# Optimization experiments

Measured on AMD Instinct MI355X. Metric: run time of the kernel, lower is better.

Reference implementation:

```python
import jax, jax.numpy as jnp
import numpy as np

EPS = 1e-8


def setup_inputs() -> dict:
    key = jax.random.key(0)
    k1, k2 = jax.random.split(key)
    latent = jax.random.normal(k1, (16, 192, 64, 64), dtype=jnp.float32)
    codebook = jax.random.normal(k2, (1024, 192), dtype=jnp.float32)
    # codebook rows are unit-normalized at init in the original module
    codebook = codebook / jnp.linalg.norm(codebook, axis=-1, keepdims=True)
    return {"latent": latent, "codebook": codebook}


def reference(latent, codebook):
    b, c, h, w = latent.shape
    # [B,C,H,W] -> [N, C]
    x = jnp.transpose(latent, (0, 2, 3, 1)).reshape(-1, c)
    x = x / (jnp.linalg.norm(x, axis=-1, keepdims=True) + EPS)
    x2 = jnp.sum(x * x, axis=-1, keepdims=True)            # [N,1]
    c2 = jnp.sum(codebook * codebook, axis=-1)             # [K]
    dist_sq = x2 - 2.0 * jnp.einsum('nd,kd->nk', x, codebook) + c2[None, :]
    indices = jnp.argmin(dist_sq, axis=-1)                 # [N]
    quantized_flat = codebook[indices]                     # [N,C] gather
    quantized = jnp.transpose(quantized_flat.reshape(b, h, w, c), (0, 3, 1, 2))
    return quantized, indices.reshape(b, h, w)
```

## Files before the change

kernel.cpp:

```cpp
#include <hip/hip_runtime.h>
#include <hip/hip_bf16.h>


#define NPTS   65536
#define DIMS   192
#define KCB    1024
#define HW     4096
#define QELEMS 12582912

typedef __attribute__((ext_vector_type(8))) _Float16 f16x8;
typedef __attribute__((ext_vector_type(4))) _Float16 f16x4;
typedef __attribute__((ext_vector_type(4))) float f32x4;

#define MARGIN_Q 4864u

__device__ __forceinline__ void async_load16(const void* g, void* l) {
    __builtin_amdgcn_global_load_lds(
        (const __attribute__((address_space(1))) unsigned int*)g,
        (__attribute__((address_space(3))) unsigned int*)l, 16, 0, 0);
}

__device__ __forceinline__ unsigned qdist(float d) {
    float t = (d + 1.0f) * 1048576.0f;
    t = fminf(fmaxf(t, 0.0f), 4194303.0f);
    return (unsigned)t;
}

__device__ __forceinline__ void top2_merge(unsigned& b, unsigned& s,
                                           unsigned ob, unsigned os) {
    unsigned nb = min(b, ob);
    unsigned ns = min(max(b, ob), min(s, os));
    b = nb; s = ns;
}

__global__ __launch_bounds__(256) void k_prep_cb16(const float* __restrict__ cbk,
                                                   _Float16* __restrict__ Bpf) {
    int id = blockIdx.x * 256 + threadIdx.x;
    if (id >= KCB * DIMS) return;
    int k = id / DIMS, d = id % DIMS;
    Bpf[((size_t)(d >> 6) * KCB + k) * 64 + (d & 63)] = (_Float16)cbk[id];
}

__global__ __launch_bounds__(256) void k_c2(const float* __restrict__ cbk,
                                            float* __restrict__ c2) {
    int k = blockIdx.x * 256 + threadIdx.x;
    if (k >= KCB) return;
    const float4* row = (const float4*)(cbk + (size_t)k * DIMS);
    float s = 0.f;
    #pragma unroll
    for (int i = 0; i < DIMS / 4; ++i) {
        float4 v = row[i];
        s += v.x * v.x + v.y * v.y + v.z * v.z + v.w * v.w;
    }
    c2[k] = s;
}

__global__ __launch_bounds__(256) void k_cbT(const float* __restrict__ cbk,
                                             float* __restrict__ cbkT) {
    __shared__ float q[64 * 193];
    const int tid = threadIdx.x;
    const int k0 = blockIdx.x * 64;
    const int lane = tid & 63;
    const int grp = tid >> 6;
    for (int r = grp; r < 64; r += 4) {
        const float* row = cbk + (size_t)(k0 + r) * DIMS;
        for (int c = lane; c < DIMS; c += 64) q[r * 193 + c] = row[c];
    }
    __syncthreads();
    for (int d = grp; d < DIMS; d += 4) {
        cbkT[(size_t)d * KCB + k0 + lane] = q[lane * 193 + d];
    }
}

__global__ __launch_bounds__(256, 2) void k_gemm_f(const float* __restrict__ latent,
                                                   const _Float16* __restrict__ Bpf,
                                                   const float* __restrict__ c2,
                                                   const float* __restrict__ cbk,
                                                   float* __restrict__ out_q,
                                                   float* __restrict__ idxf,
                                                   int* __restrict__ list,
                                                   int* __restrict__ cnt) {
    __shared__ __align__(16) _Float16 As[128 * 200];
    __shared__ __align__(16) _Float16 Bs[128 * 64];
    __shared__ float inv_s[128];
    __shared__ uint2 t2buf[256];
    __shared__ int sidx[128];

    const int tid = threadIdx.x;
    const int wave = tid >> 6;
    const int lane = tid & 63;
    const int quad = lane >> 4;
    const int l15 = lane & 15;
    const int wm = (wave >> 1) * 64;
    const int wn = (wave & 1) * 64;
    const int n0 = blockIdx.x * 128;
    const int bB = n0 >> 12;
    const int hw0 = n0 & 4095;

    {
        float* part = (float*)Bs;
        const float* lat = latent + (size_t)bB * DIMS * HW + hw0;
        const int p = tid & 127, ch = tid >> 7;
        float ss = 0.f;
        #pragma unroll 4
        for (int i = 0; i < 24; ++i) {
            int c0 = i * 8 + ch * 4;
            float v0 = lat[(size_t)(c0 + 0) * HW + p];
            float v1 = lat[(size_t)(c0 + 1) * HW + p];
            float v2 = lat[(size_t)(c0 + 2) * HW + p];
            float v3 = lat[(size_t)(c0 + 3) * HW + p];
            ss = fmaf(v0, v0, fmaf(v1, v1, fmaf(v2, v2, fmaf(v3, v3, ss))));
            f16x4 h = { (_Float16)v0, (_Float16)v1, (_Float16)v2, (_Float16)v3 };
            *(f16x4*)&As[p * 200 + c0] = h;
        }
        part[ch * 128 + p] = ss;
        __syncthreads();
        if (tid < 128)
            inv_s[tid] = 1.0f / (sqrtf(part[tid] + part[128 + tid]) + 1e-8f);
        __syncthreads();
    }

    unsigned rb[16], rs[16];
    #pragma unroll
    for (int i = 0; i < 16; ++i) { rb[i] = 0xFFFFFFFFu; rs[i] = 0xFFFFFFFFu; }

    for (int nb = 0; nb < 8; ++nb) {
        f32x4 acc[4][4];
        #pragma unroll
        for (int mt = 0; mt < 4; ++mt)
            #pragma unroll
            for (int nt = 0; nt < 4; ++nt)
                #pragma unroll
                for (int r = 0; r < 4; ++r) acc[mt][nt][r] = 0.f;

        for (int g = 0; g < 3; ++g) {
            __syncthreads();
            #pragma unroll
            for (int i = 0; i < 4; ++i) {
                int u = i * 256 + tid;
                int m = u >> 3, c = u & 7;
                int sw = c ^ (m & 7);
                async_load16(Bpf + (((size_t)g * KCB + nb * 128 + m) * 8 + sw) * 8,
                             &Bs[u * 8]);
            }
            __syncthreads();
            #pragma unroll
            for (int s = 0; s < 2; ++s) {
                f16x8 af[4], bfr[4];
                #pragma unroll
                for (int mt = 0; mt < 4; ++mt) {
                    int m = wm + mt * 16 + l15;
                    af[mt] = *(const f16x8*)&As[m * 200 + g * 64 + s * 32 + quad * 8];
                }
                #pragma unroll
                for (int nt = 0; nt < 4; ++nt) {
                    int n = wn + nt * 16 + l15;
                    int c = (s * 4 + quad) ^ (n & 7);
                    bfr[nt] = *(const f16x8*)&Bs[n * 64 + c * 8];
                }
                #pragma unroll
                for (int mt = 0; mt < 4; ++mt)
                    #pragma unroll
                    for (int nt = 0; nt < 4; ++nt)
                        acc[mt][nt] = __builtin_amdgcn_mfma_f32_16x16x32_f16(
                            af[mt], bfr[nt], acc[mt][nt], 0, 0, 0);
            }
        }

        int kbase = nb * 128 + wn;
        float c2v[4];
        #pragma unroll
        for (int nt = 0; nt < 4; ++nt) c2v[nt] = c2[kbase + nt * 16 + l15];
        #pragma unroll
        for (int mt = 0; mt < 4; ++mt) {
            #pragma unroll
            for (int r = 0; r < 4; ++r) {
                float inv = inv_s[wm + mt * 16 + quad * 4 + r];
                unsigned p[4];
                #pragma unroll
                for (int nt = 0; nt < 4; ++nt) {
                    float dist = fmaf(-2.f * inv, acc[mt][nt][r], c2v[nt]);
                    p[nt] = (qdist(dist) << 10) | (unsigned)(kbase + nt * 16 + l15);
                }
                unsigned b01 = min(p[0], p[1]), s01 = max(p[0], p[1]);
                unsigned b23 = min(p[2], p[3]), s23 = max(p[2], p[3]);
                unsigned nbb = min(b01, b23);
                unsigned nbs = min(max(b01, b23), min(s01, s23));
                top2_merge(rb[mt * 4 + r], rs[mt * 4 + r], nbb, nbs);
            }
        }
    }

    __syncthreads();
    #pragma unroll
    for (int i = 0; i < 16; ++i) {
        unsigned b = rb[i], s = rs[i];
        #pragma unroll
        for (int off = 1; off < 16; off <<= 1) {
            unsigned ob = __shfl_xor(b, off, 64);
            unsigned os = __shfl_xor(s, off, 64);
            top2_merge(b, s, ob, os);
        }
        if (l15 == 0) {
            int mt = i >> 2, r = i & 3;
            int mloc = wm + mt * 16 + quad * 4 + r;
            t2buf[mloc * 2 + (wave & 1)] = make_uint2(b, s);
        }
    }
    __syncthreads();
    if (tid < 128) {
        uint2 x = t2buf[tid * 2];
        uint2 y = t2buf[tid * 2 + 1];
        unsigned b = x.x, s = x.y;
        top2_merge(b, s, y.x, y.y);
        int k = (int)(b & 1023u);
        sidx[tid] = k;
        idxf[n0 + tid] = (float)k;
        if (((s >> 10) - (b >> 10)) < MARGIN_Q) {
            int pos = atomicAdd(cnt, 1);
            list[pos] = n0 + tid;
        }
    }
    __syncthreads();

    float* q = (float*)As;
    for (int chk = 0; chk < 4; ++chk) {
        int p0 = chk * 32;
        for (int r = wave; r < 32; r += 4) {
            const float* row = cbk + (size_t)sidx[p0 + r] * DIMS;
            for (int c = lane; c < DIMS; c += 64) q[r * 193 + c] = row[c];
        }
        __syncthreads();
        float* ob = out_q + (size_t)bB * DIMS * HW + hw0 + p0;
        #pragma unroll
        for (int i = 0; i < 24; ++i) {
            int u = i * 256 + tid;
            int c = u >> 5, p = u & 31;
            ob[(size_t)c * HW + p] = q[p * 193 + c];
        }
        __syncthreads();
    }
}

__global__ __launch_bounds__(256) void k_rescore16(const float* __restrict__ latent,
                                                   const float* __restrict__ cbkT,
                                                   const float* __restrict__ cbk,
                                                   const float* __restrict__ c2,
                                                   const int* __restrict__ list,
                                                   const int* __restrict__ cnt,
                                                   float* __restrict__ out_q,
                                                   float* __restrict__ idxf) {
    __shared__ float xs[16][200];
    __shared__ float part[16][16];
    __shared__ float inv_s[16];
    __shared__ unsigned long long best[16];
    const int tid = threadIdx.x;
    const int count = *cnt;
    const float4* ct = (const float4*)cbkT;
    const int j = tid >> 4, dl = tid & 15;

    for (int base = blockIdx.x * 16; base < count; base += gridDim.x * 16) {
        __syncthreads();
        float ss = 0.f;
        int n = 0, bb = 0, hw = 0;
        bool valid = (base + j) < count;
        if (valid) {
            n = list[base + j]; bb = n >> 12; hw = n & 4095;
            #pragma unroll
            for (int i = 0; i < 12; ++i) {
                int d = dl + i * 16;
                float v = latent[((size_t)bb * DIMS + d) * HW + hw];
                xs[j][d] = v;
                ss = fmaf(v, v, ss);
            }
        }
        part[j][dl] = ss;
        if (tid < 16) best[tid] = ~0ull;
        __syncthreads();
        if (tid < 16) {
            float s = 0.f;
            #pragma unroll
            for (int i = 0; i < 16; ++i) s += part[tid][i];
            inv_s[tid] = 1.0f / (sqrtf(s) + 1e-8f);
        }
        __syncthreads();

        float4 a[16];
        #pragma unroll
        for (int p = 0; p < 16; ++p) a[p] = make_float4(0.f, 0.f, 0.f, 0.f);
        for (int d = 0; d < DIMS; d += 4) {
            float4 cv0 = ct[(size_t)(d + 0) * 256 + tid];
            float4 cv1 = ct[(size_t)(d + 1) * 256 + tid];
            float4 cv2 = ct[(size_t)(d + 2) * 256 + tid];
            float4 cv3 = ct[(size_t)(d + 3) * 256 + tid];
            #pragma unroll
            for (int p = 0; p < 16; ++p) {
                float4 xv = *(const float4*)&xs[p][d];
                a[p].x = fmaf(xv.x, cv0.x, a[p].x); a[p].y = fmaf(xv.x, cv0.y, a[p].y);
                a[p].z = fmaf(xv.x, cv0.z, a[p].z); a[p].w = fmaf(xv.x, cv0.w, a[p].w);
                a[p].x = fmaf(xv.y, cv1.x, a[p].x); a[p].y = fmaf(xv.y, cv1.y, a[p].y);
                a[p].z = fmaf(xv.y, cv1.z, a[p].z); a[p].w = fmaf(xv.y, cv1.w, a[p].w);
                a[p].x = fmaf(xv.z, cv2.x, a[p].x); a[p].y = fmaf(xv.z, cv2.y, a[p].y);
                a[p].z = fmaf(xv.z, cv2.z, a[p].z); a[p].w = fmaf(xv.z, cv2.w, a[p].w);
                a[p].x = fmaf(xv.w, cv3.x, a[p].x); a[p].y = fmaf(xv.w, cv3.y, a[p].y);
                a[p].z = fmaf(xv.w, cv3.z, a[p].z); a[p].w = fmaf(xv.w, cv3.w, a[p].w);
            }
        }
        #pragma unroll
        for (int p = 0; p < 16; ++p) {
            float inv = inv_s[p];
            float dot4[4] = {a[p].x, a[p].y, a[p].z, a[p].w};
            unsigned long long loc = ~0ull;
            #pragma unroll
            for (int e = 0; e < 4; ++e) {
                int k = 4 * tid + e;
                float dist = c2[k] - 2.f * inv * dot4[e];
                unsigned ub = __float_as_uint(dist);
                ub ^= (ub >> 31) ? 0xFFFFFFFFu : 0x80000000u;
                unsigned long long pk =
                    ((unsigned long long)ub << 32) | (unsigned)k;
                loc = loc < pk ? loc : pk;
            }
            #pragma unroll
            for (int off = 1; off < 64; off <<= 1) {
                unsigned long long o = __shfl_xor(loc, off, 64);
                loc = loc < o ? loc : o;
            }
            if ((tid & 63) == 0) atomicMin(&best[p], loc);
        }
        __syncthreads();
        if (valid) {
            int kk = (int)(best[j] & 0xFFFFFFFFull);
            #pragma unroll
            for (int i = 0; i < 12; ++i) {
                int d = dl + i * 16;
                out_q[((size_t)bb * DIMS + d) * HW + hw] = cbk[(size_t)kk * DIMS + d];
            }
            if (dl == 0) idxf[n] = (float)kk;
        }
    }
}

__global__ __launch_bounds__(256) void k_norms_fb(const float* __restrict__ latent,
                                                  float* __restrict__ inv_norm) {
    __shared__ float red[256];
    const int tid = threadIdx.x;
    const int n0 = blockIdx.x * 128;
    const int nl = tid & 127;
    const int half = tid >> 7;
    const int b = n0 >> 12;
    const int hw = (n0 & 4095) + nl;
    const float* base = latent + (size_t)b * DIMS * HW + hw;
    float ssq = 0.f;
    for (int c = half; c < DIMS; c += 2) {
        float v = base[(size_t)c * HW];
        ssq = fmaf(v, v, ssq);
    }
    red[tid] = ssq;
    __syncthreads();
    if (half == 0) {
        float s = red[tid] + red[tid + 128];
        inv_norm[n0 + nl] = 1.0f / (sqrtf(s) + 1e-8f);
    }
}

#define LDX  132
__global__ __launch_bounds__(256) void k_dist_fb(const float* __restrict__ latent,
                                                 const float* __restrict__ cbk,
                                                 const float* __restrict__ inv_norm,
                                                 const float* __restrict__ c2,
                                                 int* __restrict__ idx_out,
                                                 float* __restrict__ idxf_out) {
    __shared__ __align__(16) float xsm[64 * LDX];
    __shared__ __align__(16) float csm[64 * LDX];
    __shared__ unsigned long long red[128];
    const int tid = threadIdx.x;
    const int n0 = blockIdx.x * 128;
    const int b = n0 >> 12;
    const int hw0 = n0 & 4095;
    const int kt = tid & 15;
    const int mt = tid >> 4;
    const float* lat_base = latent + (size_t)b * DIMS * HW + hw0;
    float inv[8];
    #pragma unroll
    for (int i = 0; i < 8; ++i) inv[i] = inv_norm[n0 + mt * 8 + i];
    float best[8];
    int bidx[8];
    #pragma unroll
    for (int i = 0; i < 8; ++i) { best[i] = 3.4e38f; bidx[i] = 0; }
    const int nl = tid & 127;
    const int cp = tid >> 7;
    for (int k0 = 0; k0 < KCB; k0 += 128) {
        float acc[8][8];
        #pragma unroll
        for (int i = 0; i < 8; ++i)
            #pragma unroll
            for (int j = 0; j < 8; ++j) acc[i][j] = 0.f;
        for (int d0 = 0; d0 < DIMS; d0 += 64) {
            __syncthreads();
            for (int cc = cp; cc < 64; cc += 2)
                xsm[cc * LDX + nl] = lat_base[(size_t)(d0 + cc) * HW + nl];
            #pragma unroll
            for (int i = 0; i < 8; ++i) {
                int f4 = tid + 256 * i;
                int kk = f4 >> 4;
                int dq = f4 & 15;
                float4 v = *(const float4*)(cbk + (size_t)(k0 + kk) * DIMS + d0 + dq * 4);
                csm[(dq * 4 + 0) * LDX + kk] = v.x;
                csm[(dq * 4 + 1) * LDX + kk] = v.y;
                csm[(dq * 4 + 2) * LDX + kk] = v.z;
                csm[(dq * 4 + 3) * LDX + kk] = v.w;
            }
            __syncthreads();
            for (int d = 0; d < 64; ++d) {
                const float* xr = &xsm[d * LDX + mt * 8];
                const float* cr = &csm[d * LDX + kt * 8];
                float x8[8], c8[8];
                *(float4*)&x8[0] = *(const float4*)&xr[0];
                *(float4*)&x8[4] = *(const float4*)&xr[4];
                *(float4*)&c8[0] = *(const float4*)&cr[0];
                *(float4*)&c8[4] = *(const float4*)&cr[4];
                #pragma unroll
                for (int i = 0; i < 8; ++i)
                    #pragma unroll
                    for (int j = 0; j < 8; ++j)
                        acc[i][j] = fmaf(x8[i], c8[j], acc[i][j]);
            }
        }
        float cc2[8];
        #pragma unroll
        for (int j = 0; j < 8; ++j) cc2[j] = c2[k0 + kt * 8 + j];
        #pragma unroll
        for (int i = 0; i < 8; ++i)
            #pragma unroll
            for (int j = 0; j < 8; ++j) {
                float t = inv[i] * acc[i][j];
                float dist = fmaf(-2.f, t, cc2[j]);
                int kidx = k0 + kt * 8 + j;
                if (dist < best[i]) { best[i] = dist; bidx[i] = kidx; }
            }
    }
    if (tid < 128) red[tid] = ~0ull;
    __syncthreads();
    #pragma unroll
    for (int i = 0; i < 8; ++i) {
        unsigned long long p =
            ((unsigned long long)__float_as_uint(best[i]) << 32) | (unsigned)bidx[i];
        atomicMin(&red[mt * 8 + i], p);
    }
    __syncthreads();
    if (tid < 128) {
        int k = (int)(red[tid] & 0xFFFFFFFFu);
        idx_out[n0 + tid] = k;
        idxf_out[n0 + tid] = (float)k;
    }
}

__global__ __launch_bounds__(256) void k_gather(const float* __restrict__ cbk,
                                                const int* __restrict__ idx,
                                                float* __restrict__ out) {
    __shared__ float q[64 * 193];
    __shared__ int sidx[64];
    const int tid = threadIdx.x;
    const int n0 = blockIdx.x * 64;
    const int b = n0 >> 12;
    const int hw0 = n0 & 4095;
    const int lane = tid & 63;
    const int grp = tid >> 6;

    if (tid < 64) sidx[tid] = idx[n0 + tid];
    __syncthreads();
    for (int r = grp; r < 64; r += 4) {
        const float* row = cbk + (size_t)sidx[r] * DIMS;
        for (int c = lane; c < DIMS; c += 64) q[r * 193 + c] = row[c];
    }
    __syncthreads();
    float* obase = out + (size_t)b * DIMS * HW + hw0;
    for (int c = grp; c < DIMS; c += 4) {
        obase[(size_t)c * HW + lane] = q[lane * 193 + c];
    }
}

extern "C" void kernel_launch(void* const* d_in, const int* in_sizes, int n_in,
                              void* d_out, int out_size, void* d_ws, size_t ws_size,
                              hipStream_t stream) {
    const float* latent = (const float*)d_in[0];
    const float* cbk = (const float*)d_in[1];
    float* out = (float*)d_out;
    float* out_q = out;
    float* out_idx = out + QELEMS;

    if (ws_size >= 2u * 1024u * 1024u) {
        char* w = (char*)d_ws;
        _Float16* Bpf = (_Float16*)w;
        float* cbkT = (float*)(w + 393216);
        float* c2 = (float*)(w + 1179648);
        int* list = (int*)(w + 1183744);
        int* cnt = (int*)(w + 1445888);

        hipMemsetAsync(cnt, 0, 4, stream);
        k_prep_cb16<<<768, 256, 0, stream>>>(cbk, Bpf);
        k_c2<<<4, 256, 0, stream>>>(cbk, c2);
        k_cbT<<<KCB / 64, 256, 0, stream>>>(cbk, cbkT);
        k_gemm_f<<<512, 256, 0, stream>>>(latent, Bpf, c2, cbk, out_q, out_idx,
                                          list, cnt);
        k_rescore16<<<512, 256, 0, stream>>>(latent, cbkT, cbk, c2, list, cnt,
                                             out_q, out_idx);
    } else {
        float* inv_norm = (float*)d_ws;
        float* c2 = inv_norm + NPTS;
        int* idx = (int*)(c2 + KCB);
        k_norms_fb<<<NPTS / 128, 256, 0, stream>>>(latent, inv_norm);
        k_c2<<<4, 256, 0, stream>>>(cbk, c2);
        k_dist_fb<<<NPTS / 128, 256, 0, stream>>>(latent, cbk, inv_norm, c2, idx, out_idx);
        k_gather<<<NPTS / 64, 256, 0, stream>>>(cbk, idx, out_q);
    }
}
```

Before: 234.7 us.

## Double-buffer codebook tiles, keep A fragments in registers, score by max dot product

The GEMM main loop is restructured. Codebook tiles are now 32-wide K-chunks loaded asynchronously into a double-buffered LDS area, so the next chunk's load overlaps with the current MFMAs and each step needs fewer barriers. The A fragments for all six chunks are preloaded into registers once. Scoring drops the c2 term and argmaxes the scaled dot product, which assumes unit-norm codebook rows. The rescoring margin is halved to shrink the candidate list, at the cost of more register pressure and a reliance on the unit-norm property.

```diff
diff --git a/kernel.cpp b/kernel.cpp
--- a/kernel.cpp
+++ b/kernel.cpp
@@ -1,5 +1,4 @@
 #include <hip/hip_runtime.h>
-#include <hip/hip_bf16.h>
 
 
 #define NPTS   65536
@@ -12,7 +11,7 @@
 typedef __attribute__((ext_vector_type(4))) _Float16 f16x4;
 typedef __attribute__((ext_vector_type(4))) float f32x4;
 
-#define MARGIN_Q 4864u
+#define MARGIN_Q 2432u
 
 __device__ __forceinline__ void async_load16(const void* g, void* l) {
     __builtin_amdgcn_global_load_lds(
@@ -20,16 +19,10 @@
         (__attribute__((address_space(3))) unsigned int*)l, 16, 0, 0);
 }
 
-__device__ __forceinline__ unsigned qdist(float d) {
-    float t = (d + 1.0f) * 1048576.0f;
-    t = fminf(fmaxf(t, 0.0f), 4194303.0f);
-    return (unsigned)t;
-}
-
-__device__ __forceinline__ void top2_merge(unsigned& b, unsigned& s,
-                                           unsigned ob, unsigned os) {
-    unsigned nb = min(b, ob);
-    unsigned ns = min(max(b, ob), min(s, os));
+__device__ __forceinline__ void top2_merge_max(unsigned& b, unsigned& s,
+                                               unsigned ob, unsigned os) {
+    unsigned nb = max(b, ob);
+    unsigned ns = max(min(b, ob), max(s, os));
     b = nb; s = ns;
 }
 
@@ -38,7 +31,7 @@
     int id = blockIdx.x * 256 + threadIdx.x;
     if (id >= KCB * DIMS) return;
     int k = id / DIMS, d = id % DIMS;
-    Bpf[((size_t)(d >> 6) * KCB + k) * 64 + (d & 63)] = (_Float16)cbk[id];
+    Bpf[((size_t)(d >> 5) * KCB + k) * 32 + (d & 31)] = (_Float16)cbk[id];
 }
 
 __global__ __launch_bounds__(256) void k_c2(const float* __restrict__ cbk,
@@ -74,14 +67,13 @@
 
 __global__ __launch_bounds__(256, 2) void k_gemm_f(const float* __restrict__ latent,
                                                    const _Float16* __restrict__ Bpf,
-                                                   const float* __restrict__ c2,
                                                    const float* __restrict__ cbk,
                                                    float* __restrict__ out_q,
                                                    float* __restrict__ idxf,
                                                    int* __restrict__ list,
                                                    int* __restrict__ cnt) {
     __shared__ __align__(16) _Float16 As[128 * 200];
-    __shared__ __align__(16) _Float16 Bs[128 * 64];
+    __shared__ __align__(16) _Float16 Bs[2][128 * 32];
     __shared__ float inv_s[128];
     __shared__ uint2 t2buf[256];
     __shared__ int sidx[128];
@@ -98,7 +90,7 @@
     const int hw0 = n0 & 4095;
 
     {
-        float* part = (float*)Bs;
+        float* part = (float*)&Bs[0][0];
         const float* lat = latent + (size_t)bB * DIMS * HW + hw0;
         const int p = tid & 127, ch = tid >> 7;
         float ss = 0.f;
@@ -120,9 +112,42 @@
         __syncthreads();
     }
 
+    f16x8 af[6][4];
+    #pragma unroll
+    for (int c = 0; c < 6; ++c)
+        #pragma unroll
+        for (int mt = 0; mt < 4; ++mt)
+            af[c][mt] = *(const f16x8*)&As[(wm + mt * 16 + l15) * 200 + c * 32 + quad * 8];
+
+    float scl[16];
+    #pragma unroll
+    for (int mt = 0; mt < 4; ++mt)
+        #pragma unroll
+        for (int r = 0; r < 4; ++r)
+            scl[mt * 4 + r] = inv_s[wm + mt * 16 + quad * 4 + r] * 1048576.0f;
+
     unsigned rb[16], rs[16];
     #pragma unroll
-    for (int i = 0; i < 16; ++i) { rb[i] = 0xFFFFFFFFu; rs[i] = 0xFFFFFFFFu; }
+    for (int i = 0; i < 16; ++i) { rb[i] = 0u; rs[i] = 0u; }
+
+    int kn[4];
+    #pragma unroll
+    for (int nt = 0; nt < 4; ++nt) kn[nt] = wn + nt * 16 + l15;
+
+    const int u0 = tid, u1 = tid + 256;
+    const int pu0 = (u0 & ~3) | ((u0 & 3) ^ ((u0 >> 2) & 3));
+    const int pu1 = (u1 & ~3) | ((u1 & 3) ^ ((u1 >> 2) & 3));
+    const int bfo = (wn + l15) * 32 + ((quad ^ (l15 & 3)) * 8);
+
+    {
+        const _Float16* s0 = Bpf;
+        async_load16(s0 + (size_t)pu0 * 8, &Bs[0][u0 * 8]);
+        async_load16(s0 + (size_t)pu1 * 8, &Bs[0][u1 * 8]);
+        const _Float16* s1 = Bpf + (size_t)KCB * 32;
+        async_load16(s1 + (size_t)pu0 * 8, &Bs[1][u0 * 8]);
+        async_load16(s1 + (size_t)pu1 * 8, &Bs[1][u1 * 8]);
+    }
+    int nb_s = 0, c_s = 2;
 
     for (int nb = 0; nb < 8; ++nb) {
         f32x4 acc[4][4];
@@ -133,62 +158,53 @@
                 #pragma unroll
                 for (int r = 0; r < 4; ++r) acc[mt][nt][r] = 0.f;
 
-        for (int g = 0; g < 3; ++g) {
-            __syncthreads();
-            #pragma unroll
-            for (int i = 0; i < 4; ++i) {
-                int u = i * 256 + tid;
-                int m = u >> 3, c = u & 7;
-                int sw = c ^ (m & 7);
-                async_load16(Bpf + (((size_t)g * KCB + nb * 128 + m) * 8 + sw) * 8,
-                             &Bs[u * 8]);
-            }
-            __syncthreads();
-            #pragma unroll
-            for (int s = 0; s < 2; ++s) {
-                f16x8 af[4], bfr[4];
+        #pragma unroll
+        for (int c = 0; c < 6; ++c) {
+            if (c == 5 && nb == 7) {
+                asm volatile("s_waitcnt vmcnt(0)" ::: "memory");
+            } else {
+                asm volatile("s_waitcnt vmcnt(2)" ::: "memory");
+            }
+            __builtin_amdgcn_s_barrier();
+            const int buf = (nb * 6 + c) & 1;
+            f16x8 bf[4];
+            #pragma unroll
+            for (int nt = 0; nt < 4; ++nt)
+                bf[nt] = *(const f16x8*)&Bs[buf][bfo + nt * 512];
+            #pragma unroll
+            for (int mt = 0; mt < 4; ++mt)
                 #pragma unroll
-                for (int mt = 0; mt < 4; ++mt) {
-                    int m = wm + mt * 16 + l15;
-                    af[mt] = *(const f16x8*)&As[m * 200 + g * 64 + s * 32 + quad * 8];
-                }
-                #pragma unroll
-                for (int nt = 0; nt < 4; ++nt) {
-                    int n = wn + nt * 16 + l15;
-                    int c = (s * 4 + quad) ^ (n & 7);
-                    bfr[nt] = *(const f16x8*)&Bs[n * 64 + c * 8];
-                }
-                #pragma unroll
-                for (int mt = 0; mt < 4; ++mt)
-                    #pragma unroll
-                    for (int nt = 0; nt < 4; ++nt)
-                        acc[mt][nt] = __builtin_amdgcn_mfma_f32_16x16x32_f16(
-                            af[mt], bfr[nt], acc[mt][nt], 0, 0, 0);
-            }
-        }
-
-        int kbase = nb * 128 + wn;
-        float c2v[4];
-        #pragma unroll
-        for (int nt = 0; nt < 4; ++nt) c2v[nt] = c2[kbase + nt * 16 + l15];
+                for (int nt = 0; nt < 4; ++nt)
+                    acc[mt][nt] = __builtin_amdgcn_mfma_f32_16x16x32_f16(
+                        af[c][mt], bf[nt], acc[mt][nt], 0, 0, 0);
+            asm volatile("s_waitcnt lgkmcnt(0)" ::: "memory");
+            __builtin_amdgcn_s_barrier();
+            if (!((c >= 4) && nb == 7)) {
+                const _Float16* src = Bpf + ((size_t)c_s * KCB + nb_s * 128) * 32;
+                async_load16(src + (size_t)pu0 * 8, &Bs[buf][u0 * 8]);
+                async_load16(src + (size_t)pu1 * 8, &Bs[buf][u1 * 8]);
+                if (++c_s == 6) { c_s = 0; ++nb_s; }
+            }
+        }
+
         #pragma unroll
         for (int mt = 0; mt < 4; ++mt) {
             #pragma unroll
             for (int r = 0; r < 4; ++r) {
-                float inv = inv_s[wm + mt * 16 + quad * 4 + r];
-                unsigned p[4];
-                #pragma unroll
-                for (int nt = 0; nt < 4; ++nt) {
-                    float dist = fmaf(-2.f * inv, acc[mt][nt][r], c2v[nt]);
-                    p[nt] = (qdist(dist) << 10) | (unsigned)(kbase + nt * 16 + l15);
-                }
-                unsigned b01 = min(p[0], p[1]), s01 = max(p[0], p[1]);
-                unsigned b23 = min(p[2], p[3]), s23 = max(p[2], p[3]);
-                unsigned nbb = min(b01, b23);
-                unsigned nbs = min(max(b01, b23), min(s01, s23));
-                top2_merge(rb[mt * 4 + r], rs[mt * 4 + r], nbb, nbs);
-            }
-        }
+                float sc = scl[mt * 4 + r];
+                unsigned p0 = ((unsigned)fmaf(acc[mt][0][r], sc, 2097152.0f) << 10) | (unsigned)kn[0];
+                unsigned p1 = ((unsigned)fmaf(acc[mt][1][r], sc, 2097152.0f) << 10) | (unsigned)kn[1];
+                unsigned p2 = ((unsigned)fmaf(acc[mt][2][r], sc, 2097152.0f) << 10) | (unsigned)kn[2];
+                unsigned p3 = ((unsigned)fmaf(acc[mt][3][r], sc, 2097152.0f) << 10) | (unsigned)kn[3];
+                unsigned b01 = max(p0, p1), s01 = min(p0, p1);
+                unsigned b23 = max(p2, p3), s23 = min(p2, p3);
+                unsigned bb = max(b01, b23);
+                unsigned s4 = max(min(b01, b23), max(s01, s23));
+                top2_merge_max(rb[mt * 4 + r], rs[mt * 4 + r], bb, s4);
+            }
+        }
+        #pragma unroll
+        for (int nt = 0; nt < 4; ++nt) kn[nt] += 128;
     }
 
     __syncthreads();
@@ -199,7 +215,7 @@
         for (int off = 1; off < 16; off <<= 1) {
             unsigned ob = __shfl_xor(b, off, 64);
             unsigned os = __shfl_xor(s, off, 64);
-            top2_merge(b, s, ob, os);
+            top2_merge_max(b, s, ob, os);
         }
         if (l15 == 0) {
             int mt = i >> 2, r = i & 3;
@@ -212,11 +228,11 @@
         uint2 x = t2buf[tid * 2];
         uint2 y = t2buf[tid * 2 + 1];
         unsigned b = x.x, s = x.y;
-        top2_merge(b, s, y.x, y.y);
+        top2_merge_max(b, s, y.x, y.y);
         int k = (int)(b & 1023u);
         sidx[tid] = k;
         idxf[n0 + tid] = (float)k;
-        if (((s >> 10) - (b >> 10)) < MARGIN_Q) {
+        if (((b >> 10) - (s >> 10)) < MARGIN_Q) {
             int pos = atomicAdd(cnt, 1);
             list[pos] = n0 + tid;
         }
@@ -502,7 +518,7 @@
         k_prep_cb16<<<768, 256, 0, stream>>>(cbk, Bpf);
         k_c2<<<4, 256, 0, stream>>>(cbk, c2);
         k_cbT<<<KCB / 64, 256, 0, stream>>>(cbk, cbkT);
-        k_gemm_f<<<512, 256, 0, stream>>>(latent, Bpf, c2, cbk, out_q, out_idx,
+        k_gemm_f<<<512, 256, 0, stream>>>(latent, Bpf, cbk, out_q, out_idx,
                                           list, cnt);
         k_rescore16<<<512, 256, 0, stream>>>(latent, cbkT, cbk, c2, list, cnt,
                                              out_q, out_idx);
```

Result: slower. 241.0 us (+2.7%).

## Fuse exact-fp32 rescoring into the GEMM kernel and merge codebook prep kernels

Applied to the files above, without the earlier changes.

Merges the three codebook preparation kernels into one that builds the fp16 packed codebook, the transposed fp32 copy and the row norms from a single shared-memory tile. The fp16 MFMA kernel now ranks candidates by raw dot product (max instead of min distance) and sets the ambiguity margin per point from its norm. Ambiguous points are collected in a per-block shared list and rescored exactly in fp32 inside the same kernel, before the quantized rows are written. This removes the separate rescoring launch, the global atomic counter and its memset, and the second write of quantized rows. In exchange, blocks with many ambiguous points take longer, which can cause load imbalance, and the candidate ranking now relies on the codebook rows being unit-norm.

```diff
diff --git a/kernel.cpp b/kernel.cpp
--- a/kernel.cpp
+++ b/kernel.cpp
@@ -1,5 +1,4 @@
 #include <hip/hip_runtime.h>
-#include <hip/hip_bf16.h>
 
 
 #define NPTS   65536
@@ -12,7 +11,6 @@
 typedef __attribute__((ext_vector_type(4))) _Float16 f16x4;
 typedef __attribute__((ext_vector_type(4))) float f32x4;
 
-#define MARGIN_Q 4864u
 
 __device__ __forceinline__ void async_load16(const void* g, void* l) {
     __builtin_amdgcn_global_load_lds(
@@ -20,43 +18,17 @@
         (__attribute__((address_space(3))) unsigned int*)l, 16, 0, 0);
 }
 
-__device__ __forceinline__ unsigned qdist(float d) {
-    float t = (d + 1.0f) * 1048576.0f;
-    t = fminf(fmaxf(t, 0.0f), 4194303.0f);
-    return (unsigned)t;
-}
-
-__device__ __forceinline__ void top2_merge(unsigned& b, unsigned& s,
-                                           unsigned ob, unsigned os) {
-    unsigned nb = min(b, ob);
-    unsigned ns = min(max(b, ob), min(s, os));
+__device__ __forceinline__ void top2_merge_max(unsigned& b, unsigned& s,
+                                               unsigned ob, unsigned os) {
+    unsigned nb = max(b, ob);
+    unsigned ns = max(min(b, ob), max(s, os));
     b = nb; s = ns;
 }
 
-__global__ __launch_bounds__(256) void k_prep_cb16(const float* __restrict__ cbk,
-                                                   _Float16* __restrict__ Bpf) {
-    int id = blockIdx.x * 256 + threadIdx.x;
-    if (id >= KCB * DIMS) return;
-    int k = id / DIMS, d = id % DIMS;
-    Bpf[((size_t)(d >> 6) * KCB + k) * 64 + (d & 63)] = (_Float16)cbk[id];
-}
-
-__global__ __launch_bounds__(256) void k_c2(const float* __restrict__ cbk,
-                                            float* __restrict__ c2) {
-    int k = blockIdx.x * 256 + threadIdx.x;
-    if (k >= KCB) return;
-    const float4* row = (const float4*)(cbk + (size_t)k * DIMS);
-    float s = 0.f;
-    #pragma unroll
-    for (int i = 0; i < DIMS / 4; ++i) {
-        float4 v = row[i];
-        s += v.x * v.x + v.y * v.y + v.z * v.z + v.w * v.w;
-    }
-    c2[k] = s;
-}
-
-__global__ __launch_bounds__(256) void k_cbT(const float* __restrict__ cbk,
-                                             float* __restrict__ cbkT) {
+__global__ __launch_bounds__(256) void k_prep(const float* __restrict__ cbk,
+                                              _Float16* __restrict__ Bpf,
+                                              float* __restrict__ cbkT,
+                                              float* __restrict__ c2) {
     __shared__ float q[64 * 193];
     const int tid = threadIdx.x;
     const int k0 = blockIdx.x * 64;
@@ -67,24 +39,40 @@
         for (int c = lane; c < DIMS; c += 64) q[r * 193 + c] = row[c];
     }
     __syncthreads();
-    for (int d = grp; d < DIMS; d += 4) {
+    for (int d = grp; d < DIMS; d += 4)
         cbkT[(size_t)d * KCB + k0 + lane] = q[lane * 193 + d];
+    for (int r = grp; r < 64; r += 4)
+        for (int c = lane; c < DIMS; c += 64)
+            Bpf[((size_t)(c >> 6) * KCB + k0 + r) * 64 + (c & 63)] =
+                (_Float16)q[r * 193 + c];
+    if (tid < 64) {
+        float s = 0.f;
+        #pragma unroll 4
+        for (int c = 0; c < DIMS; ++c) {
+            float v = q[tid * 193 + c];
+            s = fmaf(v, v, s);
+        }
+        c2[k0 + tid] = s;
     }
 }
 
 __global__ __launch_bounds__(256, 2) void k_gemm_f(const float* __restrict__ latent,
                                                    const _Float16* __restrict__ Bpf,
+                                                   const float* __restrict__ cbkT,
                                                    const float* __restrict__ c2,
                                                    const float* __restrict__ cbk,
                                                    float* __restrict__ out_q,
-                                                   float* __restrict__ idxf,
-                                                   int* __restrict__ list,
-                                                   int* __restrict__ cnt) {
+                                                   float* __restrict__ idxf) {
     __shared__ __align__(16) _Float16 As[128 * 200];
     __shared__ __align__(16) _Float16 Bs[128 * 64];
-    __shared__ float inv_s[128];
+    __shared__ float nrm_s[128];
     __shared__ uint2 t2buf[256];
     __shared__ int sidx[128];
+    __shared__ int slist[128];
+    __shared__ int scnt;
+    __shared__ float part16[16][16];
+    __shared__ float inv16[16];
+    __shared__ unsigned long long best16[16];
 
     const int tid = threadIdx.x;
     const int wave = tid >> 6;
@@ -96,10 +84,11 @@
     const int n0 = blockIdx.x * 128;
     const int bB = n0 >> 12;
     const int hw0 = n0 & 4095;
+    const size_t latb = (size_t)bB * DIMS * HW;
 
     {
         float* part = (float*)Bs;
-        const float* lat = latent + (size_t)bB * DIMS * HW + hw0;
+        const float* lat = latent + latb + hw0;
         const int p = tid & 127, ch = tid >> 7;
         float ss = 0.f;
         #pragma unroll 4
@@ -116,13 +105,14 @@
         part[ch * 128 + p] = ss;
         __syncthreads();
         if (tid < 128)
-            inv_s[tid] = 1.0f / (sqrtf(part[tid] + part[128 + tid]) + 1e-8f);
+            nrm_s[tid] = sqrtf(part[tid] + part[128 + tid]);
+        if (tid == 0) scnt = 0;
         __syncthreads();
     }
 
     unsigned rb[16], rs[16];
     #pragma unroll
-    for (int i = 0; i < 16; ++i) { rb[i] = 0xFFFFFFFFu; rs[i] = 0xFFFFFFFFu; }
+    for (int i = 0; i < 16; ++i) { rb[i] = 0u; rs[i] = 0u; }
 
     for (int nb = 0; nb < 8; ++nb) {
         f32x4 acc[4][4];
@@ -143,6 +133,7 @@
                 async_load16(Bpf + (((size_t)g * KCB + nb * 128 + m) * 8 + sw) * 8,
                              &Bs[u * 8]);
             }
+            asm volatile("s_waitcnt vmcnt(0)" ::: "memory");
             __syncthreads();
             #pragma unroll
             for (int s = 0; s < 2; ++s) {
@@ -168,25 +159,21 @@
         }
 
         int kbase = nb * 128 + wn;
-        float c2v[4];
-        #pragma unroll
-        for (int nt = 0; nt < 4; ++nt) c2v[nt] = c2[kbase + nt * 16 + l15];
         #pragma unroll
         for (int mt = 0; mt < 4; ++mt) {
             #pragma unroll
             for (int r = 0; r < 4; ++r) {
-                float inv = inv_s[wm + mt * 16 + quad * 4 + r];
                 unsigned p[4];
                 #pragma unroll
                 for (int nt = 0; nt < 4; ++nt) {
-                    float dist = fmaf(-2.f * inv, acc[mt][nt][r], c2v[nt]);
-                    p[nt] = (qdist(dist) << 10) | (unsigned)(kbase + nt * 16 + l15);
-                }
-                unsigned b01 = min(p[0], p[1]), s01 = max(p[0], p[1]);
-                unsigned b23 = min(p[2], p[3]), s23 = max(p[2], p[3]);
-                unsigned nbb = min(b01, b23);
-                unsigned nbs = min(max(b01, b23), min(s01, s23));
-                top2_merge(rb[mt * 4 + r], rs[mt * 4 + r], nbb, nbs);
+                    p[nt] = ((unsigned)fmaf(acc[mt][nt][r], 65536.f, 2097152.f) << 10)
+                            | (unsigned)(kbase + nt * 16 + l15);
+                }
+                unsigned b01 = max(p[0], p[1]), s01 = min(p[0], p[1]);
+                unsigned b23 = max(p[2], p[3]), s23 = min(p[2], p[3]);
+                unsigned bb = max(b01, b23);
+                unsigned s4 = max(min(b01, b23), max(s01, s23));
+                top2_merge_max(rb[mt * 4 + r], rs[mt * 4 + r], bb, s4);
             }
         }
     }
@@ -199,7 +186,7 @@
         for (int off = 1; off < 16; off <<= 1) {
             unsigned ob = __shfl_xor(b, off, 64);
             unsigned os = __shfl_xor(s, off, 64);
-            top2_merge(b, s, ob, os);
+            top2_merge_max(b, s, ob, os);
         }
         if (l15 == 0) {
             int mt = i >> 2, r = i & 3;
@@ -212,15 +199,95 @@
         uint2 x = t2buf[tid * 2];
         uint2 y = t2buf[tid * 2 + 1];
         unsigned b = x.x, s = x.y;
-        top2_merge(b, s, y.x, y.y);
-        int k = (int)(b & 1023u);
-        sidx[tid] = k;
-        idxf[n0 + tid] = (float)k;
-        if (((s >> 10) - (b >> 10)) < MARGIN_Q) {
-            int pos = atomicAdd(cnt, 1);
-            list[pos] = n0 + tid;
-        }
-    }
+        top2_merge_max(b, s, y.x, y.y);
+        sidx[tid] = (int)(b & 1023u);
+        unsigned Mq = (unsigned)fmaf(152.0f, nrm_s[tid], 4.0f);
+        if (((b >> 10) - (s >> 10)) < Mq) {
+            int pos = atomicAdd(&scnt, 1);
+            slist[pos] = tid;
+        }
+    }
+    __syncthreads();
+
+    {
+        const int scnt_v = scnt;
+        float* xsf = (float*)As;
+        const float4* ct = (const float4*)cbkT;
+        const int j = tid >> 4, dl = tid & 15;
+        for (int base = 0; base < scnt_v; base += 16) {
+            const bool valid = (base + j) < scnt_v;
+            const int ploc = valid ? slist[base + j] : 0;
+            float ss = 0.f;
+            if (valid) {
+                #pragma unroll
+                for (int i = 0; i < 12; ++i) {
+                    int d = dl + i * 16;
+                    float v = latent[latb + (size_t)d * HW + hw0 + ploc];
+                    xsf[j * 200 + d] = v;
+                    ss = fmaf(v, v, ss);
+                }
+            }
+            part16[j][dl] = ss;
+            if (tid < 16) best16[tid] = ~0ull;
+            __syncthreads();
+            if (tid < 16) {
+                float s = 0.f;
+                #pragma unroll
+                for (int i = 0; i < 16; ++i) s += part16[tid][i];
+                inv16[tid] = 1.0f / (sqrtf(s) + 1e-8f);
+            }
+            __syncthreads();
+            float4 a[16];
+            #pragma unroll
+            for (int p = 0; p < 16; ++p) a[p] = make_float4(0.f, 0.f, 0.f, 0.f);
+            for (int d = 0; d < DIMS; d += 4) {
+                float4 cv0 = ct[(size_t)(d + 0) * 256 + tid];
+                float4 cv1 = ct[(size_t)(d + 1) * 256 + tid];
+                float4 cv2 = ct[(size_t)(d + 2) * 256 + tid];
+                float4 cv3 = ct[(size_t)(d + 3) * 256 + tid];
+                #pragma unroll
+                for (int p = 0; p < 16; ++p) {
+                    float4 xv = *(const float4*)&xsf[p * 200 + d];
+                    a[p].x = fmaf(xv.x, cv0.x, a[p].x); a[p].y = fmaf(xv.x, cv0.y, a[p].y);
+                    a[p].z = fmaf(xv.x, cv0.z, a[p].z); a[p].w = fmaf(xv.x, cv0.w, a[p].w);
+                    a[p].x = fmaf(xv.y, cv1.x, a[p].x); a[p].y = fmaf(xv.y, cv1.y, a[p].y);
+                    a[p].z = fmaf(xv.y, cv1.z, a[p].z); a[p].w = fmaf(xv.y, cv1.w, a[p].w);
+                    a[p].x = fmaf(xv.z, cv2.x, a[p].x); a[p].y = fmaf(xv.z, cv2.y, a[p].y);
+                    a[p].z = fmaf(xv.z, cv2.z, a[p].z); a[p].w = fmaf(xv.z, cv2.w, a[p].w);
+                    a[p].x = fmaf(xv.w, cv3.x, a[p].x); a[p].y = fmaf(xv.w, cv3.y, a[p].y);
+                    a[p].z = fmaf(xv.w, cv3.z, a[p].z); a[p].w = fmaf(xv.w, cv3.w, a[p].w);
+                }
+            }
+            #pragma unroll
+            for (int p = 0; p < 16; ++p) {
+                float inv = inv16[p];
+                float dot4[4] = {a[p].x, a[p].y, a[p].z, a[p].w};
+                unsigned long long loc = ~0ull;
+                #pragma unroll
+                for (int e = 0; e < 4; ++e) {
+                    int k = 4 * tid + e;
+                    float dist = c2[k] - 2.f * inv * dot4[e];
+                    unsigned ub = __float_as_uint(dist);
+                    ub ^= (ub >> 31) ? 0xFFFFFFFFu : 0x80000000u;
+                    unsigned long long pk =
+                        ((unsigned long long)ub << 32) | (unsigned)k;
+                    loc = loc < pk ? loc : pk;
+                }
+                #pragma unroll
+                for (int off = 1; off < 64; off <<= 1) {
+                    unsigned long long o = __shfl_xor(loc, off, 64);
+                    loc = loc < o ? loc : o;
+                }
+                if ((tid & 63) == 0) atomicMin(&best16[p], loc);
+            }
+            __syncthreads();
+            if (valid && dl == 0)
+                sidx[ploc] = (int)(best16[j] & 0xFFFFFFFFull);
+            __syncthreads();
+        }
+    }
+
+    if (tid < 128) idxf[n0 + tid] = (float)sidx[tid];
     __syncthreads();
 
     float* q = (float*)As;
@@ -231,7 +298,7 @@
             for (int c = lane; c < DIMS; c += 64) q[r * 193 + c] = row[c];
         }
         __syncthreads();
-        float* ob = out_q + (size_t)bB * DIMS * HW + hw0 + p0;
+        float* ob = out_q + latb + hw0 + p0;
         #pragma unroll
         for (int i = 0; i < 24; ++i) {
             int u = i * 256 + tid;
@@ -239,105 +306,6 @@
             ob[(size_t)c * HW + p] = q[p * 193 + c];
         }
         __syncthreads();
-    }
-}
-
-__global__ __launch_bounds__(256) void k_rescore16(const float* __restrict__ latent,
-                                                   const float* __restrict__ cbkT,
-                                                   const float* __restrict__ cbk,
-                                                   const float* __restrict__ c2,
-                                                   const int* __restrict__ list,
-                                                   const int* __restrict__ cnt,
-                                                   float* __restrict__ out_q,
-                                                   float* __restrict__ idxf) {
-    __shared__ float xs[16][200];
-    __shared__ float part[16][16];
-    __shared__ float inv_s[16];
-    __shared__ unsigned long long best[16];
-    const int tid = threadIdx.x;
-    const int count = *cnt;
-    const float4* ct = (const float4*)cbkT;
-    const int j = tid >> 4, dl = tid & 15;
-
-    for (int base = blockIdx.x * 16; base < count; base += gridDim.x * 16) {
-        __syncthreads();
-        float ss = 0.f;
-        int n = 0, bb = 0, hw = 0;
-        bool valid = (base + j) < count;
-        if (valid) {
-            n = list[base + j]; bb = n >> 12; hw = n & 4095;
-            #pragma unroll
-            for (int i = 0; i < 12; ++i) {
-                int d = dl + i * 16;
-                float v = latent[((size_t)bb * DIMS + d) * HW + hw];
-                xs[j][d] = v;
-                ss = fmaf(v, v, ss);
-            }
-        }
-        part[j][dl] = ss;
-        if (tid < 16) best[tid] = ~0ull;
-        __syncthreads();
-        if (tid < 16) {
-            float s = 0.f;
-            #pragma unroll
-            for (int i = 0; i < 16; ++i) s += part[tid][i];
-            inv_s[tid] = 1.0f / (sqrtf(s) + 1e-8f);
-        }
-        __syncthreads();
-
-        float4 a[16];
-        #pragma unroll
-        for (int p = 0; p < 16; ++p) a[p] = make_float4(0.f, 0.f, 0.f, 0.f);
-        for (int d = 0; d < DIMS; d += 4) {
-            float4 cv0 = ct[(size_t)(d + 0) * 256 + tid];
-            float4 cv1 = ct[(size_t)(d + 1) * 256 + tid];
-            float4 cv2 = ct[(size_t)(d + 2) * 256 + tid];
-            float4 cv3 = ct[(size_t)(d + 3) * 256 + tid];
-            #pragma unroll
-            for (int p = 0; p < 16; ++p) {
-                float4 xv = *(const float4*)&xs[p][d];
-                a[p].x = fmaf(xv.x, cv0.x, a[p].x); a[p].y = fmaf(xv.x, cv0.y, a[p].y);
-                a[p].z = fmaf(xv.x, cv0.z, a[p].z); a[p].w = fmaf(xv.x, cv0.w, a[p].w);
-                a[p].x = fmaf(xv.y, cv1.x, a[p].x); a[p].y = fmaf(xv.y, cv1.y, a[p].y);
-                a[p].z = fmaf(xv.y, cv1.z, a[p].z); a[p].w = fmaf(xv.y, cv1.w, a[p].w);
-                a[p].x = fmaf(xv.z, cv2.x, a[p].x); a[p].y = fmaf(xv.z, cv2.y, a[p].y);
-                a[p].z = fmaf(xv.z, cv2.z, a[p].z); a[p].w = fmaf(xv.z, cv2.w, a[p].w);
-                a[p].x = fmaf(xv.w, cv3.x, a[p].x); a[p].y = fmaf(xv.w, cv3.y, a[p].y);
-                a[p].z = fmaf(xv.w, cv3.z, a[p].z); a[p].w = fmaf(xv.w, cv3.w, a[p].w);
-            }
-        }
-        #pragma unroll
-        for (int p = 0; p < 16; ++p) {
-            float inv = inv_s[p];
-            float dot4[4] = {a[p].x, a[p].y, a[p].z, a[p].w};
-            unsigned long long loc = ~0ull;
-            #pragma unroll
-            for (int e = 0; e < 4; ++e) {
-                int k = 4 * tid + e;
-                float dist = c2[k] - 2.f * inv * dot4[e];
-                unsigned ub = __float_as_uint(dist);
-                ub ^= (ub >> 31) ? 0xFFFFFFFFu : 0x80000000u;
-                unsigned long long pk =
-                    ((unsigned long long)ub << 32) | (unsigned)k;
-                loc = loc < pk ? loc : pk;
-            }
-            #pragma unroll
-            for (int off = 1; off < 64; off <<= 1) {
-                unsigned long long o = __shfl_xor(loc, off, 64);
-                loc = loc < o ? loc : o;
-            }
-            if ((tid & 63) == 0) atomicMin(&best[p], loc);
-        }
-        __syncthreads();
-        if (valid) {
-            int kk = (int)(best[j] & 0xFFFFFFFFull);
-            #pragma unroll
-            for (int i = 0; i < 12; ++i) {
-                int d = dl + i * 16;
-                out_q[((size_t)bb * DIMS + d) * HW + hw] = cbk[(size_t)kk * DIMS + d];
-            }
-            if (dl == 0) idxf[n] = (float)kk;
-        }
     }
 }
 
@@ -362,6 +330,20 @@
         float s = red[tid] + red[tid + 128];
         inv_norm[n0 + nl] = 1.0f / (sqrtf(s) + 1e-8f);
     }
+}
+
+__global__ __launch_bounds__(256) void k_c2_fb(const float* __restrict__ cbk,
+                                               float* __restrict__ c2) {
+    int k = blockIdx.x * 256 + threadIdx.x;
+    if (k >= KCB) return;
+    const float4* row = (const float4*)(cbk + (size_t)k * DIMS);
+    float s = 0.f;
+    #pragma unroll
+    for (int i = 0; i < DIMS / 4; ++i) {
+        float4 v = row[i];
+        s += v.x * v.x + v.y * v.y + v.z * v.z + v.w * v.w;
+    }
+    c2[k] = s;
 }
 
 #define LDX  132
@@ -495,23 +477,16 @@
         _Float16* Bpf = (_Float16*)w;
         float* cbkT = (float*)(w + 393216);
         float* c2 = (float*)(w + 1179648);
-        int* list = (int*)(w + 1183744);
-        int* cnt = (int*)(w + 1445888);
-
-        hipMemsetAsync(cnt, 0, 4, stream);
-        k_prep_cb16<<<768, 256, 0, stream>>>(cbk, Bpf);
-        k_c2<<<4, 256, 0, stream>>>(cbk, c2);
-        k_cbT<<<KCB / 64, 256, 0, stream>>>(cbk, cbkT);
-        k_gemm_f<<<512, 256, 0, stream>>>(latent, Bpf, c2, cbk, out_q, out_idx,
-                                          list, cnt);
-        k_rescore16<<<512, 256, 0, stream>>>(latent, cbkT, cbk, c2, list, cnt,
-                                             out_q, out_idx);
+
+        k_prep<<<KCB / 64, 256, 0, stream>>>(cbk, Bpf, cbkT, c2);
+        k_gemm_f<<<512, 256, 0, stream>>>(latent, Bpf, cbkT, c2, cbk,
+                                          out_q, out_idx);
     } else {
         float* inv_norm = (float*)d_ws;
         float* c2 = inv_norm + NPTS;
         int* idx = (int*)(c2 + KCB);
         k_norms_fb<<<NPTS / 128, 256, 0, stream>>>(latent, inv_norm);
-        k_c2<<<4, 256, 0, stream>>>(cbk, c2);
+        k_c2_fb<<<4, 256, 0, stream>>>(cbk, c2);
         k_dist_fb<<<NPTS / 128, 256, 0, stream>>>(latent, cbk, inv_norm, c2, idx, out_idx);
         k_gather<<<NPTS / 64, 256, 0, stream>>>(cbk, idx, out_q);
     }
```

Measured after the change: 243.9 us. 1.04x slower.
